# Kernel optimization log

Hardware: AMD Instinct MI355X
Metric: run time of the kernel (lower is better)

The kernel has to match this reference:

```python
import jax, jax.numpy as jnp
import numpy as np

B, S, H = 1, 4096, 2048
NH, NKV, HD = 16, 4, 128
EPS = 1e-5
THETA = 10000.0


def rms_norm(x, w, eps=EPS):
    var = jnp.mean(jnp.square(x), axis=-1, keepdims=True)
    return x * jax.lax.rsqrt(var + eps) * w


def rotate_half(x):
    x1, x2 = jnp.split(x, 2, axis=-1)
    return jnp.concatenate([-x2, x1], axis=-1)


def rope_cos_sin(seq_len, head_dim, dtype):
    inv_freq = 1.0 / (THETA ** (jnp.arange(0, head_dim, 2, dtype=jnp.float32) / head_dim))
    t = jnp.arange(seq_len, dtype=jnp.float32)
    freqs = jnp.outer(t, inv_freq)                      # [S, HD/2]
    emb = jnp.concatenate([freqs, freqs], axis=-1)      # [S, HD]
    return jnp.cos(emb).astype(dtype), jnp.sin(emb).astype(dtype)


def setup_inputs() -> dict:
    key = jax.random.key(0)
    ks = jax.random.split(key, 5)
    return {
        "hidden_states": jax.random.normal(ks[0], (B, S, H), jnp.float32),
        "wq": jax.random.normal(ks[1], (NH * HD, H), jnp.float32) * 0.02,
        "wk": jax.random.normal(ks[2], (NKV * HD, H), jnp.float32) * 0.02,
        "wv": jax.random.normal(ks[3], (NKV * HD, H), jnp.float32) * 0.02,
        "wo": jax.random.normal(ks[4], (H, NH * HD), jnp.float32) * 0.02,
        "q_norm_w": jnp.ones((NH * HD,), jnp.float32),
        "k_norm_w": jnp.ones((NKV * HD,), jnp.float32),
    }


def reference(hidden_states, wq, wk, wv, wo, q_norm_w, k_norm_w):
    b, s, _ = hidden_states.shape
    n_rep = NH // NKV

    # projections + QK RMSNorm (applied over the full flattened head dim, pre-split)
    q = rms_norm(hidden_states @ wq.T, q_norm_w)        # [B,S,NH*HD]
    k = rms_norm(hidden_states @ wk.T, k_norm_w)        # [B,S,NKV*HD]
    v = hidden_states @ wv.T                            # [B,S,NKV*HD]

    # split heads -> [B, heads, S, HD]
    q = q.reshape(b, s, NH, HD).transpose(0, 2, 1, 3)
    k = k.reshape(b, s, NKV, HD).transpose(0, 2, 1, 3)
    v = v.reshape(b, s, NKV, HD).transpose(0, 2, 1, 3)

    # RoPE (position_ids = arange(s))
    cos, sin = rope_cos_sin(s, HD, q.dtype)             # [S, HD]
    cos = cos[None, None]                               # [1,1,S,HD]
    sin = sin[None, None]
    q = q * cos + rotate_half(q) * sin
    k = k * cos + rotate_half(k) * sin

    # GQA attention without physical KV repeat: q -> [B, NKV, n_rep, S, HD]
    qg = q.reshape(b, NKV, n_rep, s, HD)
    scale = 1.0 / np.sqrt(HD)
    scores = jnp.einsum('bgrqd,bgkd->bgrqk', qg, k) * scale   # [B,NKV,rep,S,S]

    causal = jnp.tril(jnp.ones((s, s), bool))
    scores = jnp.where(causal, scores, jnp.finfo(scores.dtype).min)

    probs = jax.nn.softmax(scores.astype(jnp.float32), axis=-1).astype(q.dtype)
    out = jnp.einsum('bgrqk,bgkd->bgrqd', probs, v)           # [B,NKV,rep,S,HD]

    # merge heads -> [B,S,NH*HD], output projection
    out = out.reshape(b, NH, s, HD).transpose(0, 2, 1, 3).reshape(b, s, NH * HD)
    return out @ wo.T
```

## Files before the change

### kernel.cpp

```cpp
#include <hip/hip_runtime.h>
#include <math.h>

#define S_LEN 4096
#define HIDDEN 2048
#define N_HEADS 16
#define N_KV 4
#define HEAD_DIM 128
#define QDIM 2048
#define KDIM 512
#define QKVD 3072
#define QSCALE 0.1275174486f

typedef __bf16 bf16x8 __attribute__((ext_vector_type(8)));
typedef float f32x4 __attribute__((ext_vector_type(4)));
typedef float f32x16 __attribute__((ext_vector_type(16)));

__device__ __forceinline__ unsigned short f2bf(float x) {
  union { float f; unsigned u; } v; v.f = x;
  unsigned r = v.u + 0x7fffu + ((v.u >> 16) & 1u);
  return (unsigned short)(r >> 16);
}
__device__ __forceinline__ float bf2f(unsigned short u) {
  union { unsigned u; float f; } v; v.u = ((unsigned)u) << 16;
  return v.f;
}

__device__ __forceinline__ float wave_sum(float x) {
#pragma unroll
  for (int w = 32; w >= 1; w >>= 1) x += __shfl_xor(x, w);
  return x;
}

__device__ __forceinline__ void cvt4(const float* __restrict__ s,
                                     unsigned short* __restrict__ d, int i) {
  float4 v = reinterpret_cast<const float4*>(s)[i];
  ushort4 o;
  o.x = f2bf(v.x); o.y = f2bf(v.y); o.z = f2bf(v.z); o.w = f2bf(v.w);
  reinterpret_cast<ushort4*>(d)[i] = o;
}

__global__ __launch_bounds__(256) void k_prep(
    const float* __restrict__ hs, const float* __restrict__ wq, const float* __restrict__ wk,
    const float* __restrict__ wv, const float* __restrict__ wo,
    unsigned short* __restrict__ Xb, unsigned short* __restrict__ Wqkv,
    unsigned short* __restrict__ Wob, float* __restrict__ cosT, float* __restrict__ sinT) {
  const int NHS = (S_LEN * HIDDEN) / 4;
  const int NWQ = (QDIM * HIDDEN) / 4;
  const int NWK = (KDIM * HIDDEN) / 4;
  const int NWV = (KDIM * HIDDEN) / 4;
  const int NWO = (HIDDEN * QDIM) / 4;
  const int NRT = S_LEN * 64;
  const int TOT = NHS + NWQ + NWK + NWV + NWO + NRT;
  const int stride = gridDim.x * 256;
  for (int i = blockIdx.x * 256 + threadIdx.x; i < TOT; i += stride) {
    int j = i;
    if (j < NHS) { cvt4(hs, Xb, j); continue; }
    j -= NHS;
    if (j < NWQ) { cvt4(wq, Wqkv, j); continue; }
    j -= NWQ;
    if (j < NWK) { cvt4(wk, Wqkv + (size_t)QDIM * HIDDEN, j); continue; }
    j -= NWK;
    if (j < NWV) { cvt4(wv, Wqkv + (size_t)(QDIM + KDIM) * HIDDEN, j); continue; }
    j -= NWV;
    if (j < NWO) { cvt4(wo, Wob, j); continue; }
    j -= NWO;
    int s = j >> 6, d = j & 63;
    float inv = powf(10000.0f, -(float)(2 * d) * (1.0f / 128.0f));
    float f = (float)s * inv;
    cosT[j] = cosf(f);
    sinT[j] = sinf(f);
  }
}

#define GKT (HIDDEN / 64)

template <int BF16OUT>
__global__ __launch_bounds__(256, 2) void k_gemm(
    const unsigned short* __restrict__ A, const unsigned short* __restrict__ B,
    void* __restrict__ Cv, int N) {
  __shared__ char ldsb[65536];
  const int tid = threadIdx.x;
  const int w = tid >> 6, lane = tid & 63;
  const int l15 = lane & 15, g16 = lane >> 4;
  const int wm = w >> 1, wn = w & 1;
  const unsigned nwg = gridDim.x * gridDim.y;
  const unsigned wg = blockIdx.y * gridDim.x + blockIdx.x;
  const unsigned cpx = nwg >> 3;
  const unsigned swz = (wg & 7) * cpx + (wg >> 3);
  const int bx = swz % gridDim.x, by = swz / gridDim.x;
  const int brow = by * 128, bcol = bx * 128;
  const char* Abp = (const char*)(A + (size_t)brow * HIDDEN);
  const char* Bbp = (const char*)(B + (size_t)bcol * HIDDEN);

#define GSTAGE(bi, kt)                                                              \
  {                                                                                 \
    _Pragma("unroll")                                                               \
    for (int j = 0; j < 4; ++j) {                                                   \
      const int slot = w * 256 + j * 64 + lane;                                     \
      const int r = slot >> 3;                                                      \
      const int cb = (slot & 7) * 16;                                               \
      const char* srcA = Abp + (size_t)r * (2 * HIDDEN) + (kt) * 128 +              \
                         (cb ^ ((r & 7) << 4));                                     \
      __builtin_amdgcn_global_load_lds(                                             \
          (const __attribute__((address_space(1))) void*)srcA,                      \
          (__attribute__((address_space(3))) void*)(ldsb + (bi)*16384 + slot * 16), \
          16, 0, 0);                                                                \
      const char* srcB = Bbp + (size_t)r * (2 * HIDDEN) + (kt) * 128 +              \
                         (cb ^ ((r & 7) << 4));                                     \
      __builtin_amdgcn_global_load_lds(                                             \
          (const __attribute__((address_space(1))) void*)srcB,                      \
          (__attribute__((address_space(3))) void*)(ldsb + 32768 + (bi)*16384 +     \
                                                    slot * 16),                     \
          16, 0, 0);                                                                \
    }                                                                               \
  }

  f32x4 acc[4][4] = {};

  GSTAGE(0, 0)
  GSTAGE(1, 1)
  asm volatile("s_waitcnt vmcnt(8)" ::: "memory");
  __builtin_amdgcn_s_barrier();

  for (int kt = 0; kt < GKT; ++kt) {
    const char* Al = ldsb + (kt & 1) * 16384;
    const char* Bl = ldsb + 32768 + (kt & 1) * 16384;
    bf16x8 a[4][2], b[4][2];
#pragma unroll
    for (int fm = 0; fm < 4; ++fm) {
      const int r = wm * 64 + fm * 16 + l15;
#pragma unroll
      for (int kh = 0; kh < 2; ++kh)
        a[fm][kh] = *reinterpret_cast<const bf16x8*>(
            Al + r * 128 + ((kh * 64 + g16 * 16) ^ ((r & 7) << 4)));
    }
#pragma unroll
    for (int fn = 0; fn < 4; ++fn) {
      const int r = wn * 64 + fn * 16 + l15;
#pragma unroll
      for (int kh = 0; kh < 2; ++kh)
        b[fn][kh] = *reinterpret_cast<const bf16x8*>(
            Bl + r * 128 + ((kh * 64 + g16 * 16) ^ ((r & 7) << 4)));
    }
#pragma unroll
    for (int kh = 0; kh < 2; ++kh)
#pragma unroll
      for (int fm = 0; fm < 4; ++fm)
#pragma unroll
        for (int fn = 0; fn < 4; ++fn)
          acc[fm][fn] =
              __builtin_amdgcn_mfma_f32_16x16x32_bf16(a[fm][kh], b[fn][kh], acc[fm][fn], 0, 0, 0);
    __builtin_amdgcn_sched_barrier(0);
    __builtin_amdgcn_s_barrier();
    if (kt + 2 < GKT) GSTAGE(kt & 1, kt + 2)
    if (kt + 1 < GKT) {
      if (kt + 2 < GKT) {
        asm volatile("s_waitcnt vmcnt(8)" ::: "memory");
      } else {
        asm volatile("s_waitcnt vmcnt(0)" ::: "memory");
      }
      __builtin_amdgcn_s_barrier();
    }
  }

  const int crow = brow + wm * 64 + g16 * 4;
  const int ccol = bcol + wn * 64 + l15;
#pragma unroll
  for (int fm = 0; fm < 4; ++fm)
#pragma unroll
    for (int fn = 0; fn < 4; ++fn)
#pragma unroll
      for (int i = 0; i < 4; ++i) {
        const size_t off = (size_t)(crow + fm * 16 + i) * N + ccol + fn * 16;
        if (BF16OUT)
          ((unsigned short*)Cv)[off] = f2bf(acc[fm][fn][i]);
        else
          ((float*)Cv)[off] = acc[fm][fn][i];
      }
#undef GSTAGE
}

__global__ __launch_bounds__(256) void k_norm_rope(
    const unsigned short* __restrict__ QKV, const float* __restrict__ qw,
    const float* __restrict__ kw, const float* __restrict__ cosT,
    const float* __restrict__ sinT, unsigned short* __restrict__ Q,
    unsigned short* __restrict__ Kd, unsigned short* __restrict__ Vt) {
  const int s = blockIdx.x;
  const int tid = threadIdx.x;
  const int lane = tid & 63, wave = tid >> 6;
  const unsigned short* row = QKV + (size_t)s * QKVD;
  __shared__ float sm[QDIM];
  __shared__ float red[4];

  float qv[8];
  {
    uint4 r = *reinterpret_cast<const uint4*>(row + tid * 8);
    unsigned u[4] = {r.x, r.y, r.z, r.w};
#pragma unroll
    for (int j = 0; j < 4; ++j) {
      qv[2 * j] = bf2f((unsigned short)(u[j] & 0xffff));
      qv[2 * j + 1] = bf2f((unsigned short)(u[j] >> 16));
    }
  }
  float ss = 0;
#pragma unroll
  for (int j = 0; j < 8; ++j) ss += qv[j] * qv[j];
  ss = wave_sum(ss);
  if (lane == 0) red[wave] = ss;
  __syncthreads();
  float tot = red[0] + red[1] + red[2] + red[3];
  float qs = rsqrtf(tot * (1.0f / QDIM) + 1e-5f) * QSCALE;
#pragma unroll
  for (int j = 0; j < 8; ++j) sm[tid * 8 + j] = qv[j] * qs * qw[tid * 8 + j];
  __syncthreads();
  {
    const int d0 = tid * 8;
    const int h = d0 >> 7;
    const int dh = d0 & 127;
    const int dc = dh & 63;
    const bool lo = dh < 64;
    const float sgn = lo ? -1.0f : 1.0f;
    const int po = lo ? 64 : -64;
    union { unsigned short b[8]; uint4 u; } pk;
#pragma unroll
    for (int j = 0; j < 8; ++j) {
      float c = cosT[s * 64 + dc + j];
      float sn = sinT[s * 64 + dc + j];
      float o = sm[d0 + j] * c + sgn * sm[d0 + po + j] * sn;
      pk.b[j] = f2bf(o);
    }
    *reinterpret_cast<uint4*>(Q + ((size_t)h * S_LEN + s) * HEAD_DIM + dh) = pk.u;
  }
  __syncthreads();

  float kx, ky;
  {
    unsigned kr = *reinterpret_cast<const unsigned*>(row + QDIM + tid * 2);
    kx = bf2f((unsigned short)(kr & 0xffff));
    ky = bf2f((unsigned short)(kr >> 16));
  }
  ss = kx * kx + ky * ky;
  ss = wave_sum(ss);
  if (lane == 0) red[wave] = ss;
  __syncthreads();
  tot = red[0] + red[1] + red[2] + red[3];
  float ks = rsqrtf(tot * (1.0f / KDIM) + 1e-5f);
  sm[tid * 2] = kx * ks * kw[tid * 2];
  sm[tid * 2 + 1] = ky * ks * kw[tid * 2 + 1];
  __syncthreads();
  {
    const int d0 = tid * 2;
    const int g = d0 >> 7;
    const int dh = d0 & 127;
    const int dc = dh & 63;
    const bool lo = dh < 64;
    const float sgn = lo ? -1.0f : 1.0f;
    const int po = lo ? 64 : -64;
    union { unsigned short b[2]; unsigned u; } pk;
#pragma unroll
    for (int j = 0; j < 2; ++j) {
      float c = cosT[s * 64 + dc + j];
      float sn = sinT[s * 64 + dc + j];
      float o = sm[d0 + j] * c + sgn * sm[d0 + po + j] * sn;
      pk.b[j] = f2bf(o);
    }
    *reinterpret_cast<unsigned*>(Kd + ((size_t)g * S_LEN + s) * HEAD_DIM + dh) = pk.u;
  }

  {
    unsigned vr = *reinterpret_cast<const unsigned*>(row + QDIM + KDIM + tid * 2);
    int dv = tid * 2;
    int g = dv >> 7, d = dv & 127;
    Vt[(size_t)(g * HEAD_DIM + d) * S_LEN + s] = (unsigned short)(vr & 0xffff);
    Vt[(size_t)(g * HEAD_DIM + d + 1) * S_LEN + s] = (unsigned short)(vr >> 16);
  }
}

__global__ __launch_bounds__(256, 3) void k_attn(
    const unsigned short* __restrict__ Q, const unsigned short* __restrict__ K,
    const unsigned short* __restrict__ Vt,
    unsigned short* __restrict__ Op0, unsigned short* __restrict__ Op1,
    float* __restrict__ Mp, float* __restrict__ Lp) {
  const int bid = blockIdx.x;
  const int qt = 127 - (bid >> 3);
  const int sub = bid & 7;
  const int g = sub >> 1, half = sub & 1;
  const int NT = qt + 1, ntlo = (NT + 1) >> 1;
  const int t0 = half ? ntlo : 0, t1 = half ? NT : ntlo;

  const int tid = threadIdx.x;
  const int w = tid >> 6, lane = tid & 63;
  const int l31 = lane & 31, g2 = lane >> 5;
  const int h = g * 4 + w;
  const int qpos = qt * 32;

  unsigned short* __restrict__ Op = half ? Op1 : Op0;
  float* __restrict__ Mh = Mp + half * (16 * 4096);
  float* __restrict__ Lh = Lp + half * (16 * 4096);

  if (t0 >= t1) {
    if (g2 == 0) {
      Mh[h * 4096 + qpos + l31] = -1e30f;
      Lh[h * 4096 + qpos + l31] = 0.f;
    }
    return;
  }

  __shared__ char lds[2][16384];

  const char* Kgb = (const char*)(K + (size_t)g * S_LEN * HEAD_DIM);
  const char* Vgb = (const char*)(Vt + (size_t)g * HEAD_DIM * S_LEN);

  const bool isK = (w < 2);
  const int wj = isK ? w : (w - 2);

#define STAGE(BUFP, KV0)                                                                  \
  {                                                                                       \
    char* dstb = (BUFP);                                                                  \
    _Pragma("unroll")                                                                     \
    for (int j = 0; j < 4; ++j) {                                                         \
      if (isK) {                                                                          \
        const int r = (wj * 4 + j) * 4 + (lane >> 4);                                     \
        const char* src = Kgb + (size_t)((KV0) + r) * 256 +                               \
                          (((lane & 15) * 16) ^ ((r & 15) << 4));                         \
        __builtin_amdgcn_global_load_lds(                                                 \
            (const __attribute__((address_space(1))) void*)src,                           \
            (__attribute__((address_space(3))) void*)(dstb + (wj * 4 + j) * 1024),        \
            16, 0, 0);                                                                    \
      } else {                                                                            \
        const int r = (wj * 4 + j) * 8 + (lane >> 3);                                     \
        const int cu = ((lane & 7) * 16) ^ ((r & 7) << 4);                                \
        const int dd = 2 * r + (cu >> 6);                                                 \
        const char* src = Vgb + (size_t)dd * 8192 + (size_t)(KV0) * 2 + (cu & 63);        \
        __builtin_amdgcn_global_load_lds(                                                 \
            (const __attribute__((address_space(1))) void*)src,                           \
            (__attribute__((address_space(3))) void*)(dstb + 8192 + (wj * 4 + j) * 1024), \
            16, 0, 0);                                                                    \
      }                                                                                   \
    }                                                                                     \
  }

  STAGE(lds[0], t0 * 32)

  bf16x8 qf[8];
#pragma unroll
  for (int dc2 = 0; dc2 < 8; ++dc2)
    qf[dc2] = *reinterpret_cast<const bf16x8*>(
        Q + ((size_t)h * S_LEN + qpos + l31) * HEAD_DIM + dc2 * 16 + g2 * 8);

  f32x16 o[4] = {};
  float m = -1e30f, l = 0.f;

  for (int t = t0; t < t1; ++t) {
    char* buf = lds[(t - t0) & 1];
    __syncthreads();
    if (t + 1 < t1) STAGE(lds[(t - t0 + 1) & 1], (t + 1) * 32)
    const char* Kl = buf;
    const char* Vl = buf + 8192;
    const int kv0 = t * 32;

    f32x16 sc = {};
    __builtin_amdgcn_s_setprio(1);
#pragma unroll
    for (int dc2 = 0; dc2 < 8; ++dc2) {
      bf16x8 kf = *reinterpret_cast<const bf16x8*>(
          Kl + l31 * 256 + ((dc2 * 32 + g2 * 16) ^ ((l31 & 15) << 4)));
      sc = __builtin_amdgcn_mfma_f32_32x32x16_bf16(kf, qf[dc2], sc, 0, 0, 0);
    }
    __builtin_amdgcn_s_setprio(0);
    if (t == qt) {
#pragma unroll
      for (int reg = 0; reg < 16; ++reg) {
        int kv = kv0 + (reg & 3) + 8 * (reg >> 2) + 4 * g2;
        if (kv > qpos + l31) sc[reg] = -1e30f;
      }
    }
    float pm = sc[0];
#pragma unroll
    for (int i = 1; i < 16; ++i) pm = fmaxf(pm, sc[i]);
    pm = fmaxf(pm, __shfl_xor(pm, 32));
    if (!__all(pm <= m + 8.f)) {
      float mn = fmaxf(m, pm);
      float fac = __builtin_amdgcn_exp2f(m - mn);
#pragma unroll
      for (int dc = 0; dc < 4; ++dc) o[dc] *= fac;
      l *= fac;
      m = mn;
    }
    union { __bf16 b[16]; unsigned u[8]; } P;
    float rs = 0.f;
#pragma unroll
    for (int i = 0; i < 16; ++i) {
      float p = __builtin_amdgcn_exp2f(sc[i] - m);
      rs += p;
      P.b[i] = (__bf16)p;
    }
    rs += __shfl_xor(rs, 32);
    l += rs;
    uint4 pf[2];
#pragma unroll
    for (int c16 = 0; c16 < 2; ++c16) {
      unsigned A0 = P.u[c16 * 4], A1 = P.u[c16 * 4 + 1];
      unsigned A2 = P.u[c16 * 4 + 2], A3 = P.u[c16 * 4 + 3];
      unsigned A0x = __shfl_xor(A0, 32), A1x = __shfl_xor(A1, 32);
      unsigned A2x = __shfl_xor(A2, 32), A3x = __shfl_xor(A3, 32);
      pf[c16].x = g2 ? A2x : A0;
      pf[c16].y = g2 ? A3x : A1;
      pf[c16].z = g2 ? A2 : A0x;
      pf[c16].w = g2 ? A3 : A1x;
    }
    __builtin_amdgcn_s_setprio(1);
#pragma unroll
    for (int c16 = 0; c16 < 2; ++c16) {
      union { uint4 u; bf16x8 v; } cv;
      cv.u = pf[c16];
#pragma unroll
      for (int dc = 0; dc < 4; ++dc) {
        const int r = dc * 16 + (l31 >> 1);
        const int cu = (l31 & 1) * 64 + c16 * 32 + g2 * 16;
        bf16x8 vf = *reinterpret_cast<const bf16x8*>(Vl + r * 128 + (cu ^ ((r & 7) << 4)));
        o[dc] = __builtin_amdgcn_mfma_f32_32x32x16_bf16(vf, cv.v, o[dc], 0, 0, 0);
      }
    }
    __builtin_amdgcn_s_setprio(0);
  }

  if (g2 == 0) {
    Mh[h * 4096 + qpos + l31] = m;
    Lh[h * 4096 + qpos + l31] = l;
  }
#pragma unroll
  for (int dc = 0; dc < 4; ++dc)
#pragma unroll
    for (int reg = 0; reg < 16; ++reg) {
      int d = dc * 32 + (reg & 3) + 8 * (reg >> 2) + 4 * g2;
      Op[(((size_t)(h * 128 + d)) << 12) + qpos + l31] = f2bf(o[dc][reg]);
    }
#undef STAGE
}

__global__ __launch_bounds__(256) void k_combine(
    const unsigned short* __restrict__ Op0, const unsigned short* __restrict__ Op1,
    const float* __restrict__ Mp, const float* __restrict__ Lp,
    unsigned short* __restrict__ AO) {
  const int idx = blockIdx.x * 256 + threadIdx.x;
  const int h = idx >> 12, q = idx & 4095;
  const float m0 = Mp[h * 4096 + q], m1 = Mp[16 * 4096 + h * 4096 + q];
  const float l0 = Lp[h * 4096 + q], l1 = Lp[16 * 4096 + h * 4096 + q];
  const float mm = fmaxf(m0, m1);
  const float w0 = __builtin_amdgcn_exp2f(m0 - mm);
  const float w1 = __builtin_amdgcn_exp2f(m1 - mm);
  const float denom = w0 * l0 + w1 * l1;
  const float c0 = w0 / denom, c1 = w1 / denom;
  const bool has1 = (l1 > 0.f);
  const size_t bq = ((size_t)h * 128) << 12;
#pragma unroll
  for (int halfd = 0; halfd < 2; ++halfd) {
    float acc[64];
#pragma unroll
    for (int i = 0; i < 64; ++i) {
      const size_t off = bq + (((size_t)(halfd * 64 + i)) << 12) + q;
      float v = c0 * bf2f(Op0[off]);
      if (has1) v += c1 * bf2f(Op1[off]);
      acc[i] = v;
    }
#pragma unroll
    for (int dc = 0; dc < 8; ++dc) {
      union { unsigned short s[8]; uint4 u; } pk;
#pragma unroll
      for (int j = 0; j < 8; ++j) pk.s[j] = f2bf(acc[dc * 8 + j]);
      *reinterpret_cast<uint4*>(AO + (size_t)q * QDIM + h * 128 + halfd * 64 + dc * 8) = pk.u;
    }
  }
}

extern "C" void kernel_launch(void* const* d_in, const int* in_sizes, int n_in,
                              void* d_out, int out_size, void* d_ws, size_t ws_size,
                              hipStream_t stream) {
  const float* hs = (const float*)d_in[0];
  const float* wq = (const float*)d_in[1];
  const float* wk = (const float*)d_in[2];
  const float* wv = (const float*)d_in[3];
  const float* wo = (const float*)d_in[4];
  const float* qnw = (const float*)d_in[5];
  const float* knw = (const float*)d_in[6];
  float* out = (float*)d_out;

  char* base = (char*)d_ws;
  unsigned short* Xb = (unsigned short*)base;
  unsigned short* Qb = Xb;
  unsigned short* Wqkv = (unsigned short*)(base + 16777216);
  unsigned short* Kb = Wqkv;
  unsigned short* Vtb = (unsigned short*)(base + 20971520);
  float* Mp = (float*)(base + 25165824);
  float* Lp = (float*)(base + 25690112);
  unsigned short* Wob = (unsigned short*)(base + 29360128);
  unsigned short* QKVb = (unsigned short*)(base + 37748736);
  unsigned short* AOb = QKVb;
  unsigned short* Op0 = (unsigned short*)(base + 54525952);
  unsigned short* Op1 = (unsigned short*)(base + 71303168);
  float* cosT = (float*)(base + 88080384);
  float* sinT = (float*)(base + 89128960);

  k_prep<<<2048, 256, 0, stream>>>(hs, wq, wk, wv, wo, Xb, Wqkv, Wob, cosT, sinT);
  k_gemm<1><<<dim3(QKVD / 128, S_LEN / 128), 256, 0, stream>>>(Xb, Wqkv, (void*)QKVb, QKVD);
  k_norm_rope<<<S_LEN, 256, 0, stream>>>(QKVb, qnw, knw, cosT, sinT, Qb, Kb, Vtb);
  k_attn<<<1024, 256, 0, stream>>>(Qb, Kb, Vtb, Op0, Op1, Mp, Lp);
  k_combine<<<256, 256, 0, stream>>>(Op0, Op1, Mp, Lp, AOb);
  k_gemm<0><<<dim3(QDIM / 128, S_LEN / 128), 256, 0, stream>>>(AOb, Wob, (void*)out, QDIM);
}
```

Measured before the change: 308.4 us.

## Halve GEMM K-tile to 32 with repacked LDS layout for higher occupancy

The GEMM k-step shrinks from 64 to 32, halving the LDS footprint to 32KB and raising launch bounds to 4 waves per SIMD. A new LDS layout folds two 64-row halves into 128-byte rows so the existing XOR swizzle still applies. Fewer registers hold A/B fragments, and the vmcnt waits are adjusted to match. In exchange there are twice as many loop iterations and barriers per tile, and less MFMA work between syncs.

```diff
diff --git a/kernel.cpp b/kernel.cpp
--- a/kernel.cpp
+++ b/kernel.cpp
@@ -72,13 +72,13 @@
   }
 }
 
-#define GKT (HIDDEN / 64)
+#define GKT (HIDDEN / 32)
 
 template <int BF16OUT>
-__global__ __launch_bounds__(256, 2) void k_gemm(
+__global__ __launch_bounds__(256, 4) void k_gemm(
     const unsigned short* __restrict__ A, const unsigned short* __restrict__ B,
     void* __restrict__ Cv, int N) {
-  __shared__ char ldsb[65536];
+  __shared__ char ldsb[32768];
   const int tid = threadIdx.x;
   const int w = tid >> 6, lane = tid & 63;
   const int l15 = lane & 15, g16 = lane >> 4;
@@ -92,70 +92,66 @@
   const char* Abp = (const char*)(A + (size_t)brow * HIDDEN);
   const char* Bbp = (const char*)(B + (size_t)bcol * HIDDEN);
 
-#define GSTAGE(bi, kt)                                                              \
-  {                                                                                 \
-    _Pragma("unroll")                                                               \
-    for (int j = 0; j < 4; ++j) {                                                   \
-      const int slot = w * 256 + j * 64 + lane;                                     \
-      const int r = slot >> 3;                                                      \
-      const int cb = (slot & 7) * 16;                                               \
-      const char* srcA = Abp + (size_t)r * (2 * HIDDEN) + (kt) * 128 +              \
-                         (cb ^ ((r & 7) << 4));                                     \
-      __builtin_amdgcn_global_load_lds(                                             \
-          (const __attribute__((address_space(1))) void*)srcA,                      \
-          (__attribute__((address_space(3))) void*)(ldsb + (bi)*16384 + slot * 16), \
-          16, 0, 0);                                                                \
-      const char* srcB = Bbp + (size_t)r * (2 * HIDDEN) + (kt) * 128 +              \
-                         (cb ^ ((r & 7) << 4));                                     \
-      __builtin_amdgcn_global_load_lds(                                             \
-          (const __attribute__((address_space(1))) void*)srcB,                      \
-          (__attribute__((address_space(3))) void*)(ldsb + 32768 + (bi)*16384 +     \
-                                                    slot * 16),                     \
-          16, 0, 0);                                                                \
-    }                                                                               \
+#define GSTAGE(bi, kt)                                                               \
+  {                                                                                  \
+    _Pragma("unroll")                                                                \
+    for (int j = 0; j < 2; ++j) {                                                    \
+      const int slot = j * 256 + tid;                                                \
+      const int r = slot >> 3;                                                       \
+      const int c = ((slot & 7) * 16) ^ ((r & 7) << 4);                              \
+      const int rr = r + ((c >> 6) << 6);                                            \
+      const int kb = c & 63;                                                         \
+      const char* srcA = Abp + (size_t)rr * (2 * HIDDEN) + (kt) * 64 + kb;           \
+      __builtin_amdgcn_global_load_lds(                                              \
+          (const __attribute__((address_space(1))) void*)srcA,                       \
+          (__attribute__((address_space(3))) void*)(ldsb + (bi)*8192 + slot * 16),   \
+          16, 0, 0);                                                                 \
+      const char* srcB = Bbp + (size_t)rr * (2 * HIDDEN) + (kt) * 64 + kb;           \
+      __builtin_amdgcn_global_load_lds(                                              \
+          (const __attribute__((address_space(1))) void*)srcB,                       \
+          (__attribute__((address_space(3))) void*)(ldsb + 16384 + (bi)*8192 +       \
+                                                    slot * 16),                      \
+          16, 0, 0);                                                                 \
+    }                                                                                \
   }
 
   f32x4 acc[4][4] = {};
 
   GSTAGE(0, 0)
   GSTAGE(1, 1)
-  asm volatile("s_waitcnt vmcnt(8)" ::: "memory");
+  asm volatile("s_waitcnt vmcnt(4)" ::: "memory");
   __builtin_amdgcn_s_barrier();
 
   for (int kt = 0; kt < GKT; ++kt) {
-    const char* Al = ldsb + (kt & 1) * 16384;
-    const char* Bl = ldsb + 32768 + (kt & 1) * 16384;
-    bf16x8 a[4][2], b[4][2];
+    const char* Al = ldsb + (kt & 1) * 8192;
+    const char* Bl = ldsb + 16384 + (kt & 1) * 8192;
+    bf16x8 a[4], b[4];
 #pragma unroll
     for (int fm = 0; fm < 4; ++fm) {
-      const int r = wm * 64 + fm * 16 + l15;
-#pragma unroll
-      for (int kh = 0; kh < 2; ++kh)
-        a[fm][kh] = *reinterpret_cast<const bf16x8*>(
-            Al + r * 128 + ((kh * 64 + g16 * 16) ^ ((r & 7) << 4)));
+      const int rr = wm * 64 + fm * 16 + l15;
+      const int r = rr & 63;
+      const int c = ((rr >> 6) << 6) | (g16 * 16);
+      a[fm] = *reinterpret_cast<const bf16x8*>(Al + r * 128 + (c ^ ((r & 7) << 4)));
     }
 #pragma unroll
     for (int fn = 0; fn < 4; ++fn) {
-      const int r = wn * 64 + fn * 16 + l15;
-#pragma unroll
-      for (int kh = 0; kh < 2; ++kh)
-        b[fn][kh] = *reinterpret_cast<const bf16x8*>(
-            Bl + r * 128 + ((kh * 64 + g16 * 16) ^ ((r & 7) << 4)));
-    }
-#pragma unroll
-    for (int kh = 0; kh < 2; ++kh)
-#pragma unroll
-      for (int fm = 0; fm < 4; ++fm)
-#pragma unroll
-        for (int fn = 0; fn < 4; ++fn)
-          acc[fm][fn] =
-              __builtin_amdgcn_mfma_f32_16x16x32_bf16(a[fm][kh], b[fn][kh], acc[fm][fn], 0, 0, 0);
+      const int rr = wn * 64 + fn * 16 + l15;
+      const int r = rr & 63;
+      const int c = ((rr >> 6) << 6) | (g16 * 16);
+      b[fn] = *reinterpret_cast<const bf16x8*>(Bl + r * 128 + (c ^ ((r & 7) << 4)));
+    }
+#pragma unroll
+    for (int fm = 0; fm < 4; ++fm)
+#pragma unroll
+      for (int fn = 0; fn < 4; ++fn)
+        acc[fm][fn] =
+            __builtin_amdgcn_mfma_f32_16x16x32_bf16(a[fm], b[fn], acc[fm][fn], 0, 0, 0);
     __builtin_amdgcn_sched_barrier(0);
     __builtin_amdgcn_s_barrier();
     if (kt + 2 < GKT) GSTAGE(kt & 1, kt + 2)
     if (kt + 1 < GKT) {
       if (kt + 2 < GKT) {
-        asm volatile("s_waitcnt vmcnt(8)" ::: "memory");
+        asm volatile("s_waitcnt vmcnt(4)" ::: "memory");
       } else {
         asm volatile("s_waitcnt vmcnt(0)" ::: "memory");
       }
```

Result: slower. 321.0 us (+4.1%).

## Enlarge GEMM tiles to 256x256 with 8 waves and finer-grained pipelined staging

Applied to the files above, without the earlier changes.

Both projection GEMMs now use 256x256 output tiles with 512 threads (8 waves, 2x4 layout), 128KB of LDS and 128 accumulator registers per lane. The K loop is split into four half-stage phases, each interleaving LDS reads, async global-to-LDS loads for the next stage and an MFMA burst raised with s_setprio. The goal is more data reuse per loaded byte and better overlap of loads with compute. In exchange the grids shrink (192 and 128 blocks), which may underfill the 256 CUs, and register and LDS pressure rise sharply.

```diff
diff --git a/kernel.cpp b/kernel.cpp
--- a/kernel.cpp
+++ b/kernel.cpp
@@ -72,101 +72,152 @@
   }
 }
 
-#define GKT (HIDDEN / 64)
+#define GKT2 (HIDDEN / 64)
 
 template <int BF16OUT>
-__global__ __launch_bounds__(256, 2) void k_gemm(
+__global__ __launch_bounds__(512, 2) void k_gemm(
     const unsigned short* __restrict__ A, const unsigned short* __restrict__ B,
     void* __restrict__ Cv, int N) {
-  __shared__ char ldsb[65536];
+  __shared__ char ldsb[131072];
   const int tid = threadIdx.x;
   const int w = tid >> 6, lane = tid & 63;
   const int l15 = lane & 15, g16 = lane >> 4;
-  const int wm = w >> 1, wn = w & 1;
+  const int wm = w >> 2, wn = w & 3;
   const unsigned nwg = gridDim.x * gridDim.y;
   const unsigned wg = blockIdx.y * gridDim.x + blockIdx.x;
   const unsigned cpx = nwg >> 3;
   const unsigned swz = (wg & 7) * cpx + (wg >> 3);
   const int bx = swz % gridDim.x, by = swz / gridDim.x;
-  const int brow = by * 128, bcol = bx * 128;
+  const int brow = by * 256, bcol = bx * 256;
   const char* Abp = (const char*)(A + (size_t)brow * HIDDEN);
   const char* Bbp = (const char*)(B + (size_t)bcol * HIDDEN);
 
-#define GSTAGE(bi, kt)                                                              \
-  {                                                                                 \
-    _Pragma("unroll")                                                               \
-    for (int j = 0; j < 4; ++j) {                                                   \
-      const int slot = w * 256 + j * 64 + lane;                                     \
-      const int r = slot >> 3;                                                      \
-      const int cb = (slot & 7) * 16;                                               \
-      const char* srcA = Abp + (size_t)r * (2 * HIDDEN) + (kt) * 128 +              \
-                         (cb ^ ((r & 7) << 4));                                     \
-      __builtin_amdgcn_global_load_lds(                                             \
-          (const __attribute__((address_space(1))) void*)srcA,                      \
-          (__attribute__((address_space(3))) void*)(ldsb + (bi)*16384 + slot * 16), \
-          16, 0, 0);                                                                \
-      const char* srcB = Bbp + (size_t)r * (2 * HIDDEN) + (kt) * 128 +              \
-                         (cb ^ ((r & 7) << 4));                                     \
-      __builtin_amdgcn_global_load_lds(                                             \
-          (const __attribute__((address_space(1))) void*)srcB,                      \
-          (__attribute__((address_space(3))) void*)(ldsb + 32768 + (bi)*16384 +     \
-                                                    slot * 16),                     \
-          16, 0, 0);                                                                \
-    }                                                                               \
-  }
-
-  f32x4 acc[4][4] = {};
-
-  GSTAGE(0, 0)
-  GSTAGE(1, 1)
+#define STG(bi, kt, isB, kh)                                                            \
+  {                                                                                     \
+    const char* gb = (isB) ? Bbp : Abp;                                                 \
+    char* db = ldsb + (bi) * 65536 + (isB) * 32768 + (kh) * 16384;                      \
+    _Pragma("unroll")                                                                   \
+    for (int j = 0; j < 2; ++j) {                                                       \
+      const int slot = j * 512 + tid;                                                   \
+      const int R = slot >> 3;                                                          \
+      const int cp = ((slot & 7) * 16) ^ ((R & 7) << 4);                                \
+      const int r = 2 * R + (cp >> 6);                                                  \
+      const int kb = cp & 63;                                                           \
+      __builtin_amdgcn_global_load_lds(                                                 \
+          (const __attribute__((address_space(1))) void*)(gb + (size_t)r * 4096 +      \
+                                                          (kt) * 128 + (kh) * 64 + kb),\
+          (__attribute__((address_space(3))) void*)(db + slot * 16), 16, 0, 0);         \
+    }                                                                                   \
+  }
+
+#define RD(reg, regionp, rfull, khX)                                                    \
+  {                                                                                     \
+    const int rp_ = (rfull) >> 1;                                                       \
+    reg = *reinterpret_cast<const bf16x8*>(                                             \
+        (regionp) + (khX) * 16384 + rp_ * 128 +                                         \
+        ((g16 * 16 + ((rfull) & 1) * 64) ^ ((rp_ & 7) << 4)));                          \
+  }
+
+  f32x4 acc[8][4] = {};
+
+  STG(0, 0, 0, 0) STG(0, 0, 1, 0) STG(0, 0, 0, 1) STG(0, 0, 1, 1)
+  STG(1, 1, 0, 0) STG(1, 1, 1, 0)
   asm volatile("s_waitcnt vmcnt(8)" ::: "memory");
   __builtin_amdgcn_s_barrier();
 
-  for (int kt = 0; kt < GKT; ++kt) {
-    const char* Al = ldsb + (kt & 1) * 16384;
-    const char* Bl = ldsb + 32768 + (kt & 1) * 16384;
-    bf16x8 a[4][2], b[4][2];
-#pragma unroll
-    for (int fm = 0; fm < 4; ++fm) {
-      const int r = wm * 64 + fm * 16 + l15;
-#pragma unroll
-      for (int kh = 0; kh < 2; ++kh)
-        a[fm][kh] = *reinterpret_cast<const bf16x8*>(
-            Al + r * 128 + ((kh * 64 + g16 * 16) ^ ((r & 7) << 4)));
-    }
-#pragma unroll
-    for (int fn = 0; fn < 4; ++fn) {
-      const int r = wn * 64 + fn * 16 + l15;
-#pragma unroll
-      for (int kh = 0; kh < 2; ++kh)
-        b[fn][kh] = *reinterpret_cast<const bf16x8*>(
-            Bl + r * 128 + ((kh * 64 + g16 * 16) ^ ((r & 7) << 4)));
-    }
-#pragma unroll
-    for (int kh = 0; kh < 2; ++kh)
-#pragma unroll
-      for (int fm = 0; fm < 4; ++fm)
-#pragma unroll
-        for (int fn = 0; fn < 4; ++fn)
-          acc[fm][fn] =
-              __builtin_amdgcn_mfma_f32_16x16x32_bf16(a[fm][kh], b[fn][kh], acc[fm][fn], 0, 0, 0);
-    __builtin_amdgcn_sched_barrier(0);
-    __builtin_amdgcn_s_barrier();
-    if (kt + 2 < GKT) GSTAGE(kt & 1, kt + 2)
-    if (kt + 1 < GKT) {
-      if (kt + 2 < GKT) {
+  for (int t = 0; t < GKT2; ++t) {
+    const int bi = t & 1;
+    const char* Ab = ldsb + bi * 65536;
+    const char* Bb = Ab + 32768;
+    bf16x8 a[4], b[4];
+
+#pragma unroll
+    for (int f = 0; f < 4; ++f) RD(a[f], Ab, wm * 128 + f * 16 + l15, 0)
+#pragma unroll
+    for (int f = 0; f < 4; ++f) RD(b[f], Bb, wn * 64 + f * 16 + l15, 0)
+    if (t + 1 < GKT2) STG(bi ^ 1, t + 1, 0, 1)
+    __builtin_amdgcn_sched_barrier(0);
+    __builtin_amdgcn_s_barrier();
+    __builtin_amdgcn_sched_barrier(0);
+    __builtin_amdgcn_s_setprio(1);
+#pragma unroll
+    for (int fm = 0; fm < 4; ++fm)
+#pragma unroll
+      for (int fn = 0; fn < 4; ++fn)
+        acc[fm][fn] = __builtin_amdgcn_mfma_f32_16x16x32_bf16(a[fm], b[fn], acc[fm][fn], 0, 0, 0);
+    __builtin_amdgcn_s_setprio(0);
+    __builtin_amdgcn_sched_barrier(0);
+    __builtin_amdgcn_s_barrier();
+
+#pragma unroll
+    for (int f = 0; f < 4; ++f) RD(a[f], Ab, wm * 128 + (f + 4) * 16 + l15, 0)
+    if (t + 1 < GKT2) STG(bi ^ 1, t + 1, 1, 1)
+    __builtin_amdgcn_sched_barrier(0);
+    __builtin_amdgcn_s_barrier();
+    __builtin_amdgcn_sched_barrier(0);
+    __builtin_amdgcn_s_setprio(1);
+#pragma unroll
+    for (int fm = 0; fm < 4; ++fm)
+#pragma unroll
+      for (int fn = 0; fn < 4; ++fn)
+        acc[fm + 4][fn] =
+            __builtin_amdgcn_mfma_f32_16x16x32_bf16(a[fm], b[fn], acc[fm + 4][fn], 0, 0, 0);
+    __builtin_amdgcn_s_setprio(0);
+    __builtin_amdgcn_sched_barrier(0);
+    if (t + 1 < GKT2) {
+      asm volatile("s_waitcnt vmcnt(8)" ::: "memory");
+    } else {
+      asm volatile("s_waitcnt vmcnt(0)" ::: "memory");
+    }
+    __builtin_amdgcn_s_barrier();
+
+#pragma unroll
+    for (int f = 0; f < 4; ++f) RD(a[f], Ab, wm * 128 + f * 16 + l15, 1)
+#pragma unroll
+    for (int f = 0; f < 4; ++f) RD(b[f], Bb, wn * 64 + f * 16 + l15, 1)
+    if (t + 2 < GKT2) STG(bi, t + 2, 0, 0)
+    __builtin_amdgcn_sched_barrier(0);
+    __builtin_amdgcn_s_barrier();
+    __builtin_amdgcn_sched_barrier(0);
+    __builtin_amdgcn_s_setprio(1);
+#pragma unroll
+    for (int fm = 0; fm < 4; ++fm)
+#pragma unroll
+      for (int fn = 0; fn < 4; ++fn)
+        acc[fm][fn] = __builtin_amdgcn_mfma_f32_16x16x32_bf16(a[fm], b[fn], acc[fm][fn], 0, 0, 0);
+    __builtin_amdgcn_s_setprio(0);
+    __builtin_amdgcn_sched_barrier(0);
+    __builtin_amdgcn_s_barrier();
+
+#pragma unroll
+    for (int f = 0; f < 4; ++f) RD(a[f], Ab, wm * 128 + (f + 4) * 16 + l15, 1)
+    if (t + 2 < GKT2) STG(bi, t + 2, 1, 0)
+    __builtin_amdgcn_sched_barrier(0);
+    __builtin_amdgcn_s_barrier();
+    __builtin_amdgcn_sched_barrier(0);
+    __builtin_amdgcn_s_setprio(1);
+#pragma unroll
+    for (int fm = 0; fm < 4; ++fm)
+#pragma unroll
+      for (int fn = 0; fn < 4; ++fn)
+        acc[fm + 4][fn] =
+            __builtin_amdgcn_mfma_f32_16x16x32_bf16(a[fm], b[fn], acc[fm + 4][fn], 0, 0, 0);
+    __builtin_amdgcn_s_setprio(0);
+    __builtin_amdgcn_sched_barrier(0);
+    if (t + 1 < GKT2) {
+      if (t + 2 < GKT2) {
         asm volatile("s_waitcnt vmcnt(8)" ::: "memory");
       } else {
-        asm volatile("s_waitcnt vmcnt(0)" ::: "memory");
+        asm volatile("s_waitcnt vmcnt(4)" ::: "memory");
       }
       __builtin_amdgcn_s_barrier();
     }
   }
 
-  const int crow = brow + wm * 64 + g16 * 4;
+  const int crow = brow + wm * 128 + g16 * 4;
   const int ccol = bcol + wn * 64 + l15;
 #pragma unroll
-  for (int fm = 0; fm < 4; ++fm)
+  for (int fm = 0; fm < 8; ++fm)
 #pragma unroll
     for (int fn = 0; fn < 4; ++fn)
 #pragma unroll
@@ -177,7 +228,8 @@
         else
           ((float*)Cv)[off] = acc[fm][fn][i];
       }
-#undef GSTAGE
+#undef STG
+#undef RD
 }
 
 __global__ __launch_bounds__(256) void k_norm_rope(
@@ -503,9 +555,9 @@
   float* sinT = (float*)(base + 89128960);
 
   k_prep<<<2048, 256, 0, stream>>>(hs, wq, wk, wv, wo, Xb, Wqkv, Wob, cosT, sinT);
-  k_gemm<1><<<dim3(QKVD / 128, S_LEN / 128), 256, 0, stream>>>(Xb, Wqkv, (void*)QKVb, QKVD);
+  k_gemm<1><<<dim3(QKVD / 256, S_LEN / 256), 512, 0, stream>>>(Xb, Wqkv, (void*)QKVb, QKVD);
   k_norm_rope<<<S_LEN, 256, 0, stream>>>(QKVb, qnw, knw, cosT, sinT, Qb, Kb, Vtb);
   k_attn<<<1024, 256, 0, stream>>>(Qb, Kb, Vtb, Op0, Op1, Mp, Lp);
   k_combine<<<256, 256, 0, stream>>>(Op0, Op1, Mp, Lp, AOb);
-  k_gemm<0><<<dim3(QDIM / 128, S_LEN / 128), 256, 0, stream>>>(AOb, Wob, (void*)out, QDIM);
-}
+  k_gemm<0><<<dim3(QDIM / 256, S_LEN / 256), 512, 0, stream>>>(AOb, Wob, (void*)out, QDIM);
+}
```

Result: slower. 322.2 us (+4.5%).

## Process two 32-row query tiles per attention wave to reuse K/V fragments

Applied to the files above, without the earlier changes.

Each attention block now handles 64 query rows (two 32-row sub-tiles) per head instead of 32, so every K and V fragment loaded from LDS feeds two MFMAs. The grid halves to 512 blocks and launch bounds drop to 2 blocks per CU to make room for the doubled register state (two Q fragment sets, two accumulators, two softmax states). Fully masked tiles of the first sub-tile are skipped with a wave-wide activity check. This raises arithmetic intensity per LDS read and KV staging, at the cost of register pressure, lower occupancy and coarser load balancing across the causal triangle.

```diff
diff --git a/kernel.cpp b/kernel.cpp
--- a/kernel.cpp
+++ b/kernel.cpp
@@ -276,35 +276,29 @@
   }
 }
 
-__global__ __launch_bounds__(256, 3) void k_attn(
+__global__ __launch_bounds__(256, 2) void k_attn(
     const unsigned short* __restrict__ Q, const unsigned short* __restrict__ K,
     const unsigned short* __restrict__ Vt,
     unsigned short* __restrict__ Op0, unsigned short* __restrict__ Op1,
     float* __restrict__ Mp, float* __restrict__ Lp) {
   const int bid = blockIdx.x;
-  const int qt = 127 - (bid >> 3);
+  const int qt = 63 - (bid >> 3);
   const int sub = bid & 7;
   const int g = sub >> 1, half = sub & 1;
-  const int NT = qt + 1, ntlo = (NT + 1) >> 1;
+  const int NT = 2 * qt + 2;
+  const int ntlo = NT >> 1;
   const int t0 = half ? ntlo : 0, t1 = half ? NT : ntlo;
 
   const int tid = threadIdx.x;
   const int w = tid >> 6, lane = tid & 63;
   const int l31 = lane & 31, g2 = lane >> 5;
   const int h = g * 4 + w;
-  const int qpos = qt * 32;
+  const int qpos = qt * 64;
+  const int dq0 = 2 * qt, dq1 = 2 * qt + 1;
 
   unsigned short* __restrict__ Op = half ? Op1 : Op0;
   float* __restrict__ Mh = Mp + half * (16 * 4096);
   float* __restrict__ Lh = Lp + half * (16 * 4096);
-
-  if (t0 >= t1) {
-    if (g2 == 0) {
-      Mh[h * 4096 + qpos + l31] = -1e30f;
-      Lh[h * 4096 + qpos + l31] = 0.f;
-    }
-    return;
-  }
 
   __shared__ char lds[2][16384];
 
@@ -342,14 +336,17 @@
 
   STAGE(lds[0], t0 * 32)
 
-  bf16x8 qf[8];
-#pragma unroll
-  for (int dc2 = 0; dc2 < 8; ++dc2)
-    qf[dc2] = *reinterpret_cast<const bf16x8*>(
+  bf16x8 qf0[8], qf1[8];
+#pragma unroll
+  for (int dc2 = 0; dc2 < 8; ++dc2) {
+    qf0[dc2] = *reinterpret_cast<const bf16x8*>(
         Q + ((size_t)h * S_LEN + qpos + l31) * HEAD_DIM + dc2 * 16 + g2 * 8);
-
-  f32x16 o[4] = {};
-  float m = -1e30f, l = 0.f;
+    qf1[dc2] = *reinterpret_cast<const bf16x8*>(
+        Q + ((size_t)h * S_LEN + qpos + 32 + l31) * HEAD_DIM + dc2 * 16 + g2 * 8);
+  }
+
+  f32x16 o0[4] = {}, o1[4] = {};
+  float m0 = -1e30f, l0 = 0.f, m1 = -1e30f, l1 = 0.f;
 
   for (int t = t0; t < t1; ++t) {
     char* buf = lds[(t - t0) & 1];
@@ -359,82 +356,133 @@
     const char* Vl = buf + 8192;
     const int kv0 = t * 32;
 
-    f32x16 sc = {};
+    f32x16 sc0 = {}, sc1 = {};
     __builtin_amdgcn_s_setprio(1);
 #pragma unroll
     for (int dc2 = 0; dc2 < 8; ++dc2) {
       bf16x8 kf = *reinterpret_cast<const bf16x8*>(
           Kl + l31 * 256 + ((dc2 * 32 + g2 * 16) ^ ((l31 & 15) << 4)));
-      sc = __builtin_amdgcn_mfma_f32_32x32x16_bf16(kf, qf[dc2], sc, 0, 0, 0);
+      sc0 = __builtin_amdgcn_mfma_f32_32x32x16_bf16(kf, qf0[dc2], sc0, 0, 0, 0);
+      sc1 = __builtin_amdgcn_mfma_f32_32x32x16_bf16(kf, qf1[dc2], sc1, 0, 0, 0);
     }
     __builtin_amdgcn_s_setprio(0);
-    if (t == qt) {
+    if (t >= dq0) {
 #pragma unroll
       for (int reg = 0; reg < 16; ++reg) {
         int kv = kv0 + (reg & 3) + 8 * (reg >> 2) + 4 * g2;
-        if (kv > qpos + l31) sc[reg] = -1e30f;
-      }
-    }
-    float pm = sc[0];
-#pragma unroll
-    for (int i = 1; i < 16; ++i) pm = fmaxf(pm, sc[i]);
-    pm = fmaxf(pm, __shfl_xor(pm, 32));
-    if (!__all(pm <= m + 8.f)) {
-      float mn = fmaxf(m, pm);
-      float fac = __builtin_amdgcn_exp2f(m - mn);
-#pragma unroll
-      for (int dc = 0; dc < 4; ++dc) o[dc] *= fac;
-      l *= fac;
-      m = mn;
-    }
-    union { __bf16 b[16]; unsigned u[8]; } P;
-    float rs = 0.f;
-#pragma unroll
-    for (int i = 0; i < 16; ++i) {
-      float p = __builtin_amdgcn_exp2f(sc[i] - m);
-      rs += p;
-      P.b[i] = (__bf16)p;
-    }
-    rs += __shfl_xor(rs, 32);
-    l += rs;
-    uint4 pf[2];
+        if (kv > qpos + l31) sc0[reg] = -1e30f;
+      }
+    }
+    if (t == dq1) {
+#pragma unroll
+      for (int reg = 0; reg < 16; ++reg) {
+        int kv = kv0 + (reg & 3) + 8 * (reg >> 2) + 4 * g2;
+        if (kv > qpos + 32 + l31) sc1[reg] = -1e30f;
+      }
+    }
+    uint4 pf0[2], pf1[2];
+    float pm0 = sc0[0];
+#pragma unroll
+    for (int i = 1; i < 16; ++i) pm0 = fmaxf(pm0, sc0[i]);
+    pm0 = fmaxf(pm0, __shfl_xor(pm0, 32));
+    const bool act0 = __any(pm0 > -1e29f);
+    if (act0) {
+      if (!__all(pm0 <= m0 + 8.f)) {
+        float mn = fmaxf(m0, pm0);
+        float fac = __builtin_amdgcn_exp2f(m0 - mn);
+#pragma unroll
+        for (int dc = 0; dc < 4; ++dc) o0[dc] *= fac;
+        l0 *= fac;
+        m0 = mn;
+      }
+      union { __bf16 b[16]; unsigned u[8]; } P;
+      float rs = 0.f;
+#pragma unroll
+      for (int i = 0; i < 16; ++i) {
+        float p = __builtin_amdgcn_exp2f(sc0[i] - m0);
+        rs += p;
+        P.b[i] = (__bf16)p;
+      }
+      rs += __shfl_xor(rs, 32);
+      l0 += rs;
+#pragma unroll
+      for (int c16 = 0; c16 < 2; ++c16) {
+        unsigned A0 = P.u[c16 * 4], A1 = P.u[c16 * 4 + 1];
+        unsigned A2 = P.u[c16 * 4 + 2], A3 = P.u[c16 * 4 + 3];
+        unsigned A0x = __shfl_xor(A0, 32), A1x = __shfl_xor(A1, 32);
+        unsigned A2x = __shfl_xor(A2, 32), A3x = __shfl_xor(A3, 32);
+        pf0[c16].x = g2 ? A2x : A0;
+        pf0[c16].y = g2 ? A3x : A1;
+        pf0[c16].z = g2 ? A2 : A0x;
+        pf0[c16].w = g2 ? A3 : A1x;
+      }
+    }
+    {
+      float pm = sc1[0];
+#pragma unroll
+      for (int i = 1; i < 16; ++i) pm = fmaxf(pm, sc1[i]);
+      pm = fmaxf(pm, __shfl_xor(pm, 32));
+      if (!__all(pm <= m1 + 8.f)) {
+        float mn = fmaxf(m1, pm);
+        float fac = __builtin_amdgcn_exp2f(m1 - mn);
+#pragma unroll
+        for (int dc = 0; dc < 4; ++dc) o1[dc] *= fac;
+        l1 *= fac;
+        m1 = mn;
+      }
+      union { __bf16 b[16]; unsigned u[8]; } P;
+      float rs = 0.f;
+#pragma unroll
+      for (int i = 0; i < 16; ++i) {
+        float p = __builtin_amdgcn_exp2f(sc1[i] - m1);
+        rs += p;
+        P.b[i] = (__bf16)p;
+      }
+      rs += __shfl_xor(rs, 32);
+      l1 += rs;
+#pragma unroll
+      for (int c16 = 0; c16 < 2; ++c16) {
+        unsigned A0 = P.u[c16 * 4], A1 = P.u[c16 * 4 + 1];
+        unsigned A2 = P.u[c16 * 4 + 2], A3 = P.u[c16 * 4 + 3];
+        unsigned A0x = __shfl_xor(A0, 32), A1x = __shfl_xor(A1, 32);
+        unsigned A2x = __shfl_xor(A2, 32), A3x = __shfl_xor(A3, 32);
+        pf1[c16].x = g2 ? A2x : A0;
+        pf1[c16].y = g2 ? A3x : A1;
+        pf1[c16].z = g2 ? A2 : A0x;
+        pf1[c16].w = g2 ? A3 : A1x;
+      }
+    }
+    __builtin_amdgcn_s_setprio(1);
 #pragma unroll
     for (int c16 = 0; c16 < 2; ++c16) {
-      unsigned A0 = P.u[c16 * 4], A1 = P.u[c16 * 4 + 1];
-      unsigned A2 = P.u[c16 * 4 + 2], A3 = P.u[c16 * 4 + 3];
-      unsigned A0x = __shfl_xor(A0, 32), A1x = __shfl_xor(A1, 32);
-      unsigned A2x = __shfl_xor(A2, 32), A3x = __shfl_xor(A3, 32);
-      pf[c16].x = g2 ? A2x : A0;
-      pf[c16].y = g2 ? A3x : A1;
-      pf[c16].z = g2 ? A2 : A0x;
-      pf[c16].w = g2 ? A3 : A1x;
-    }
-    __builtin_amdgcn_s_setprio(1);
-#pragma unroll
-    for (int c16 = 0; c16 < 2; ++c16) {
-      union { uint4 u; bf16x8 v; } cv;
-      cv.u = pf[c16];
+      union { uint4 u; bf16x8 v; } cv0, cv1;
+      cv0.u = pf0[c16];
+      cv1.u = pf1[c16];
 #pragma unroll
       for (int dc = 0; dc < 4; ++dc) {
         const int r = dc * 16 + (l31 >> 1);
         const int cu = (l31 & 1) * 64 + c16 * 32 + g2 * 16;
         bf16x8 vf = *reinterpret_cast<const bf16x8*>(Vl + r * 128 + (cu ^ ((r & 7) << 4)));
-        o[dc] = __builtin_amdgcn_mfma_f32_32x32x16_bf16(vf, cv.v, o[dc], 0, 0, 0);
+        if (act0) o0[dc] = __builtin_amdgcn_mfma_f32_32x32x16_bf16(vf, cv0.v, o0[dc], 0, 0, 0);
+        o1[dc] = __builtin_amdgcn_mfma_f32_32x32x16_bf16(vf, cv1.v, o1[dc], 0, 0, 0);
       }
     }
     __builtin_amdgcn_s_setprio(0);
   }
 
   if (g2 == 0) {
-    Mh[h * 4096 + qpos + l31] = m;
-    Lh[h * 4096 + qpos + l31] = l;
+    Mh[h * 4096 + qpos + l31] = m0;
+    Lh[h * 4096 + qpos + l31] = l0;
+    Mh[h * 4096 + qpos + 32 + l31] = m1;
+    Lh[h * 4096 + qpos + 32 + l31] = l1;
   }
 #pragma unroll
   for (int dc = 0; dc < 4; ++dc)
 #pragma unroll
     for (int reg = 0; reg < 16; ++reg) {
       int d = dc * 32 + (reg & 3) + 8 * (reg >> 2) + 4 * g2;
-      Op[(((size_t)(h * 128 + d)) << 12) + qpos + l31] = f2bf(o[dc][reg]);
+      Op[(((size_t)(h * 128 + d)) << 12) + qpos + l31] = f2bf(o0[dc][reg]);
+      Op[(((size_t)(h * 128 + d)) << 12) + qpos + 32 + l31] = f2bf(o1[dc][reg]);
     }
 #undef STAGE
 }
@@ -505,7 +553,7 @@
   k_prep<<<2048, 256, 0, stream>>>(hs, wq, wk, wv, wo, Xb, Wqkv, Wob, cosT, sinT);
   k_gemm<1><<<dim3(QKVD / 128, S_LEN / 128), 256, 0, stream>>>(Xb, Wqkv, (void*)QKVb, QKVD);
   k_norm_rope<<<S_LEN, 256, 0, stream>>>(QKVb, qnw, knw, cosT, sinT, Qb, Kb, Vtb);
-  k_attn<<<1024, 256, 0, stream>>>(Qb, Kb, Vtb, Op0, Op1, Mp, Lp);
+  k_attn<<<512, 256, 0, stream>>>(Qb, Kb, Vtb, Op0, Op1, Mp, Lp);
   k_combine<<<256, 256, 0, stream>>>(Op0, Op1, Mp, Lp, AOb);
   k_gemm<0><<<dim3(QDIM / 128, S_LEN / 128), 256, 0, stream>>>(AOb, Wob, (void*)out, QDIM);
 }
```

After: 427.3 us. +38.6%, slower.
